# Kernel tuning notes

Hardware: AMD Instinct MI355X
Metric: run time of the kernel (lower is better)

The kernel has to match this reference:

```python
import jax, jax.numpy as jnp
import numpy as np

T_HID, A_HID, V_HID = 256, 128, 128
LEN = T_HID + A_HID + V_HID            # 512
TIME_WINDOW = 2
EXT_DIM = TIME_WINDOW * LEN + 1        # 1025
RANK, OUT_DIM = 128, 16
STRIDE = 2
B, T = 256, 128
T_IN, A_IN, V_IN = 768, 74, 35


def _mk_lstm(key, d_in, h):
    k1, k2, k3 = jax.random.split(key, 3)
    s = 1.0 / np.sqrt(h)
    W_ih = jax.random.uniform(k1, (4 * h, d_in), jnp.float32, -s, s)
    W_hh = jax.random.uniform(k2, (4 * h, h), jnp.float32, -s, s)
    b = jax.random.uniform(k3, (4 * h,), jnp.float32, -s, s)
    return W_ih, W_hh, b


def setup_inputs() -> dict:
    key = jax.random.key(0)
    ks = jax.random.split(key, 10)
    inp = {
        "text_x": jax.random.normal(ks[0], (B, T, T_IN), jnp.float32),
        "audio_x": jax.random.normal(ks[1], (B, T, A_IN), jnp.float32),
        "video_x": jax.random.normal(ks[2], (B, T, V_IN), jnp.float32),
    }
    inp["W_ih_t"], inp["W_hh_t"], inp["b_t"] = _mk_lstm(ks[3], T_IN, T_HID)
    inp["W_ih_a"], inp["W_hh_a"], inp["b_a"] = _mk_lstm(ks[4], A_IN, A_HID)
    inp["W_ih_v"], inp["W_hh_v"], inp["b_v"] = _mk_lstm(ks[5], V_IN, V_HID)
    ro = RANK * OUT_DIM
    inp["W1"] = jax.random.normal(ks[6], (ro, LEN), jnp.float32) / np.sqrt(LEN)
    inp["b1"] = jnp.zeros((ro,), jnp.float32)
    inp["W2"] = jax.random.normal(ks[7], (ro, EXT_DIM), jnp.float32) / np.sqrt(EXT_DIM)
    inp["b2"] = jnp.zeros((ro,), jnp.float32)
    inp["fusion_w"] = jax.random.normal(ks[8], (1, RANK), jnp.float32) * np.sqrt(2.0 / (1 + RANK))
    return inp


def _lstm(x, W_ih, W_hh, b, h):
    # x: [B,T,D] -> all hidden states [B,T,H]; PyTorch gate order i,f,g,o
    xp = jnp.einsum('btd,gd->btg', x, W_ih) + b  # [B,T,4H]
    h0 = jnp.zeros((x.shape[0], h), x.dtype)

    def step(carry, xt):
        hp, cp = carry
        g = xt + hp @ W_hh.T
        i, f, gg, o = jnp.split(g, 4, axis=-1)
        c = jax.nn.sigmoid(f) * cp + jax.nn.sigmoid(i) * jnp.tanh(gg)
        hn = jax.nn.sigmoid(o) * jnp.tanh(c)
        return (hn, c), hn

    _, hs = jax.lax.scan(step, (h0, h0), jnp.swapaxes(xp, 0, 1))
    return jnp.swapaxes(hs, 0, 1)


def reference(text_x, audio_x, video_x,
              W_ih_t, W_hh_t, b_t, W_ih_a, W_hh_a, b_a, W_ih_v, W_hh_v, b_v,
              W1, b1, W2, b2, fusion_w):
    audio_h = _lstm(audio_x, W_ih_a, W_hh_a, b_a, A_HID)
    video_h = _lstm(video_x, W_ih_v, W_hh_v, b_v, V_HID)
    text_h = _lstm(text_x, W_ih_t, W_hh_t, b_t, T_HID)
    z = jnp.concatenate((audio_h, video_h, text_h), axis=2)  # [B,T,LEN]

    # time_extend with circular wraparound: [B,T,1+W*LEN]
    tidx = (jnp.arange(T)[:, None] + jnp.arange(TIME_WINDOW)[None, :]) % T  # [T,W]
    z_ext = z[:, tidx, :].reshape(z.shape[0], T, TIME_WINDOW * LEN)
    ones = jnp.ones((z.shape[0], T, 1), z.dtype)
    z_ext = jnp.concatenate((ones, z_ext), axis=2)  # [B,T,EXT_DIM]

    idx = jnp.arange(0, T, STRIDE)  # strided fusion steps
    zi = z[:, idx, :]               # [B,K,LEN]
    ze = z_ext[:, idx, :]           # [B,K,EXT_DIM]
    f1 = jnp.einsum('bkd,rd->bkr', zi, W1) + b1
    f2 = jnp.einsum('bkd,rd->bkr', ze, W2) + b2
    z_fusion = jnp.mean(f1 * f2, axis=1)  # sum_i (.)/len(idx)  -> [B, RANK*OUT]
    z_fusion = z_fusion.reshape(-1, RANK, OUT_DIM)
    output = jnp.einsum('r,bro->bo', fusion_w[0], z_fusion)
    return output
```

## Files before the change

### kernel.cpp

```cpp
#include <hip/hip_runtime.h>
#include <hip/hip_bf16.h>
#include <math.h>


typedef __attribute__((ext_vector_type(8))) short short8;
typedef __attribute__((ext_vector_type(4))) float f32x4;

__device__ __forceinline__ float sigm(float x) { return 1.0f / (1.0f + __expf(-x)); }
__device__ __forceinline__ float tanh_(float x) {
    float ax = fabsf(x);
    float e  = __expf(-2.0f * ax);
    float t  = (1.0f - e) / (1.0f + e);
    return copysignf(t, x);
}
__device__ __forceinline__ ushort f2bf(float x) {
    __hip_bfloat16 h = __float2bfloat16(x);
    return *reinterpret_cast<ushort*>(&h);
}
__device__ __forceinline__ float bf2f(ushort u) { return __uint_as_float(((unsigned)u) << 16); }

__device__ __forceinline__ void gl_lds16(const void* g, void* l) {
    __builtin_amdgcn_global_load_lds(
        (const __attribute__((address_space(1))) unsigned int*)g,
        (__attribute__((address_space(3))) unsigned int*)l, 16, 0, 0);
}

#define BARRIER_LIGHT() \
    do { asm volatile("s_waitcnt lgkmcnt(0)" ::: "memory"); \
         __builtin_amdgcn_s_barrier(); \
         asm volatile("" ::: "memory"); } while (0)

__global__ void cvt_bf16(const float* __restrict__ src, ushort* __restrict__ dst,
                         int n8)
{
    int i = blockIdx.x * 256 + threadIdx.x;
    if (i >= n8) return;
    float4 a = ((const float4*)src)[2 * i];
    float4 b = ((const float4*)src)[2 * i + 1];
    short8 o;
    o[0] = f2bf(a.x); o[1] = f2bf(a.y); o[2] = f2bf(a.z); o[3] = f2bf(a.w);
    o[4] = f2bf(b.x); o[5] = f2bf(b.y); o[6] = f2bf(b.z); o[7] = f2bf(b.w);
    ((short8*)dst)[i] = o;
}

__global__ __launch_bounds__(256) void gemm_mfma_b(
    const ushort* __restrict__ A, const ushort* __restrict__ W,
    const float* __restrict__ bias, ushort* __restrict__ C,
    int M, int N, int K)
{
    constexpr int STR = 40;
    __shared__ ushort As[128 * STR];
    __shared__ ushort Ws[128 * STR];

    const int tid  = threadIdx.x;
    const int lane = tid & 63;
    const int wave = tid >> 6;
    const int bm   = blockIdx.y * 128;
    const int bn   = blockIdx.x * 128;
    const int m0   = (wave >> 1) * 64;
    const int n0   = (wave & 1) * 64;
    const int row  = tid >> 1;
    const int kseg = (tid & 1) * 16;
    const int fr   = lane & 15;
    const int fk   = (lane >> 4) * 8;

    f32x4 acc[4][4];
#pragma unroll
    for (int i = 0; i < 4; ++i)
#pragma unroll
        for (int j = 0; j < 4; ++j) acc[i][j] = (f32x4)(0.f);

    const bool kvec = (K & 7) == 0;

    for (int k0 = 0; k0 < K; k0 += 32) {
        {
            const ushort* ap = A + (size_t)(bm + row) * K + k0 + kseg;
            if (kvec && (k0 + kseg + 16) <= K) {
                *(int4*)&As[row * STR + kseg]     = *(const int4*)ap;
                *(int4*)&As[row * STR + kseg + 8] = *(const int4*)(ap + 8);
            } else {
#pragma unroll
                for (int j = 0; j < 16; ++j) {
                    int kk = k0 + kseg + j;
                    As[row * STR + kseg + j] = (kk < K) ? ap[j] : (ushort)0;
                }
            }
        }
        {
            const ushort* wp = W + (size_t)(bn + row) * K + k0 + kseg;
            if (kvec && (k0 + kseg + 16) <= K) {
                *(int4*)&Ws[row * STR + kseg]     = *(const int4*)wp;
                *(int4*)&Ws[row * STR + kseg + 8] = *(const int4*)(wp + 8);
            } else {
#pragma unroll
                for (int j = 0; j < 16; ++j) {
                    int kk = k0 + kseg + j;
                    Ws[row * STR + kseg + j] = (kk < K) ? wp[j] : (ushort)0;
                }
            }
        }
        __syncthreads();

        short8 af[4], wf[4];
#pragma unroll
        for (int mi = 0; mi < 4; ++mi)
            af[mi] = *(const short8*)&As[(m0 + mi * 16 + fr) * STR + fk];
#pragma unroll
        for (int ni = 0; ni < 4; ++ni)
            wf[ni] = *(const short8*)&Ws[(n0 + ni * 16 + fr) * STR + fk];
#pragma unroll
        for (int mi = 0; mi < 4; ++mi)
#pragma unroll
            for (int ni = 0; ni < 4; ++ni)
                acc[mi][ni] = __builtin_amdgcn_mfma_f32_16x16x32_bf16(
                    af[mi], wf[ni], acc[mi][ni], 0, 0, 0);
        __syncthreads();
    }

#pragma unroll
    for (int ni = 0; ni < 4; ++ni) {
        const int col = bn + n0 + ni * 16 + fr;
        const float bb = bias[col];
#pragma unroll
        for (int mi = 0; mi < 4; ++mi)
#pragma unroll
            for (int q = 0; q < 4; ++q) {
                int r  = bm + m0 + mi * 16 + (lane >> 4) * 4 + q;
                int b  = r >> 7, t = r & 127;
                size_t idx;
                if (N == 1024) {
                    int g = col >> 8, w = (col >> 5) & 7, s = (col >> 4) & 1, pl = col & 15;
                    idx = ((((size_t)(b >> 4) * 128 + t) * 8 + w) * 8 + (g * 2 + s)) * 256
                        + (size_t)(b & 15) * 16 + pl;
                } else {
                    int g = col >> 7, wq = (col >> 4) & 7, pl = col & 15;
                    idx = ((((size_t)(b >> 4) * 128 + t) * 8 + wq) * 4 + g) * 256
                        + (size_t)(b & 15) * 16 + pl;
                }
                C[idx] = f2bf(acc[mi][ni][q] + bb);
            }
    }
}

__global__ void wfrag_pack(const float* __restrict__ Wt, const float* __restrict__ Wa,
                           const float* __restrict__ Wv, ushort* __restrict__ WFt,
                           ushort* __restrict__ WFa, ushort* __restrict__ WFv)
{
    int idx = blockIdx.x * 256 + threadIdx.x;
    if (idx < 262144) {
        int e = idx;
        int jj = e & 7, n = (e >> 3) & 15, k8 = (e >> 7) & 3;
        int ti = e >> 9;
        int gs = ti & 7, w = (ti >> 3) & 7, kt = ti >> 6;
        int g = gs >> 1, s = gs & 1;
        WFt[e] = f2bf(Wt[(size_t)(g * 256 + w * 32 + s * 16 + n) * 256 + kt * 32 + k8 * 8 + jj]);
    } else if (idx < 327680) {
        int e = idx - 262144;
        int jj = e & 7, k8 = (e >> 3) & 3, n = (e >> 5) & 15;
        int g = (e >> 9) & 3, w = (e >> 11) & 7, kt = (e >> 14) & 3;
        WFa[e] = f2bf(Wa[(size_t)(g * 128 + w * 16 + n) * 128 + kt * 32 + k8 * 8 + jj]);
    } else if (idx < 393216) {
        int e = idx - 327680;
        int jj = e & 7, k8 = (e >> 3) & 3, n = (e >> 5) & 15;
        int g = (e >> 9) & 3, w = (e >> 11) & 7, kt = (e >> 14) & 3;
        WFv[e] = f2bf(Wv[(size_t)(g * 128 + w * 16 + n) * 128 + kt * 32 + k8 * 8 + jj]);
    }
}

__global__ void wf_pack(const float* __restrict__ W1, const float* __restrict__ W2,
                        ushort* __restrict__ W1b, ushort* __restrict__ W2ab,
                        ushort* __restrict__ W2bb)
{
    int idx = blockIdx.x * 256 + threadIdx.x;
    if (idx >= 1048576) return;
    int r = idx >> 9, c = idx & 511;
    W1b[idx]  = f2bf(W1[idx]);
    W2ab[idx] = f2bf(W2[(size_t)r * 1025 + 1 + c]);
    W2bb[idx] = f2bf(W2[(size_t)r * 1025 + 513 + c]);
}

#define STAGE_W(KT)                                                                \
    do {                                                                           \
        const char* gs_ = (const char*)WFt + (size_t)(((KT) * 8 + w) * 8) * 1024   \
                          + lane * 16;                                             \
        char* ld_ = wbuf + ((KT) & 1) * 8192;                                      \
        _Pragma("unroll") for (int e_ = 0; e_ < 8; ++e_)                           \
            gl_lds16(gs_ + e_ * 1024, ld_ + e_ * 1024);                            \
    } while (0)

#define TEXT_STEP(T, XC, XN, RP)                                                   \
    do {                                                                           \
        f32x4 acc[8];                                                              \
        _Pragma("unroll") for (int e = 0; e < 8; ++e) acc[e] = (f32x4)(0.f);       \
        _Pragma("unroll") for (int kt = 0; kt < 8; ++kt) {                         \
            if (kt < 2) { asm volatile("s_waitcnt vmcnt(16)" ::: "memory"); }      \
            else        { asm volatile("s_waitcnt vmcnt(8)" ::: "memory"); }       \
            __builtin_amdgcn_sched_barrier(0);                                     \
            short8 wt[8];                                                          \
            _Pragma("unroll") for (int e = 0; e < 8; ++e)                          \
                wt[e] = *(const short8*)(wbuf + (kt & 1) * 8192 + e * 1024 + lane * 16); \
            short8 hfk;                                                           \
            { int byt = (RP) * 8192 + np * 512 + kt * 64 + k8 * 16;                \
              hfk = *(const short8*)(hbase + (byt ^ ((np & 7) << 4))); }           \
            asm volatile("s_waitcnt lgkmcnt(0)" ::: "memory");                     \
            __builtin_amdgcn_sched_barrier(0);                                     \
            STAGE_W((kt + 2) & 7);                                                 \
            __builtin_amdgcn_sched_barrier(0);                                     \
            _Pragma("unroll") for (int e = 0; e < 8; ++e)                          \
                acc[e] = __builtin_amdgcn_mfma_f32_16x16x32_bf16(wt[e], hfk, acc[e], 0, 0, 0); \
        }                                                                          \
        _Pragma("unroll") for (int e = 0; e < 8; ++e) {                            \
            acc[e][0] += bf2f((ushort)((XC)[e].x & 0xffffu));                      \
            acc[e][1] += bf2f((ushort)((XC)[e].x >> 16));                          \
            acc[e][2] += bf2f((ushort)((XC)[e].y & 0xffffu));                      \
            acc[e][3] += bf2f((ushort)((XC)[e].y >> 16));                          \
        }                                                                          \
        uint2 hw[2];                                                               \
        _Pragma("unroll") for (int s = 0; s < 2; ++s) {                            \
            ushort hq[4];                                                          \
            _Pragma("unroll") for (int q = 0; q < 4; ++q) {                        \
                float iv = acc[0 + s][q], fv = acc[2 + s][q];                      \
                float gv = acc[4 + s][q], ov = acc[6 + s][q];                      \
                float cc = sigm(fv) * c_st[s][q] + sigm(iv) * tanh_(gv);           \
                c_st[s][q] = cc;                                                   \
                hq[q] = f2bf(sigm(ov) * tanh_(cc));                                \
            }                                                                      \
            hw[s].x = (uint)hq[0] | ((uint)hq[1] << 16);                           \
            hw[s].y = (uint)hq[2] | ((uint)hq[3] << 16);                           \
        }                                                                          \
        __builtin_amdgcn_sched_barrier(0);                                         \
        _Pragma("unroll") for (int s = 0; s < 2; ++s) {                            \
            int byt = ((RP) ^ 1) * 8192 + np * 512 + w * 64 + s * 32 + k8 * 8;     \
            *(uint2*)(hbase + (byt ^ ((np & 7) << 4))) = hw[s];                    \
            *(uint2*)(zb + zrow + (size_t)(T) * 512 + s * 16) = hw[s];             \
        }                                                                          \
        { const ushort* xrn = xbase + (size_t)(((T) + 1) & 127) * 16384;           \
          _Pragma("unroll") for (int e = 0; e < 8; ++e)                            \
              (XN)[e] = *(const uint2*)(xrn + e * 256); }                          \
        __builtin_amdgcn_sched_barrier(0);                                         \
        BARRIER_LIGHT();                                                           \
    } while (0)

#define AV_STEP(T, XC, XN, RP)                                                     \
    do {                                                                           \
        short8 hf[4];                                                              \
        _Pragma("unroll") for (int kt = 0; kt < 4; ++kt) {                         \
            int byt = (RP) * 4096 + np * 256 + kt * 64 + k8 * 16;                  \
            hf[kt] = *(const short8*)(hbase + (byt ^ ((np & 7) << 4)));            \
        }                                                                          \
        f32x4 acc[4];                                                              \
        _Pragma("unroll") for (int g = 0; g < 4; ++g) acc[g] = (f32x4)(0.f);       \
        _Pragma("unroll") for (int kt = 0; kt < 4; ++kt)                           \
            _Pragma("unroll") for (int g = 0; g < 4; ++g)                          \
                acc[g] = __builtin_amdgcn_mfma_f32_16x16x32_bf16(wres[kt][g], hf[kt], acc[g], 0, 0, 0); \
        { const ushort* xrn = xbase + (size_t)(((T) + 1) & 127) * 8192;            \
          _Pragma("unroll") for (int g = 0; g < 4; ++g)                            \
              (XN)[g] = *(const uint2*)(xrn + g * 256); }                          \
        _Pragma("unroll") for (int g = 0; g < 4; ++g) {                            \
            acc[g][0] += bf2f((ushort)((XC)[g].x & 0xffffu));                      \
            acc[g][1] += bf2f((ushort)((XC)[g].x >> 16));                          \
            acc[g][2] += bf2f((ushort)((XC)[g].y & 0xffffu));                      \
            acc[g][3] += bf2f((ushort)((XC)[g].y >> 16));                          \
        }                                                                          \
        ushort hq[4];                                                              \
        _Pragma("unroll") for (int q = 0; q < 4; ++q) {                            \
            float cc = sigm(acc[1][q]) * c_st0[q] + sigm(acc[0][q]) * tanh_(acc[2][q]); \
            c_st0[q] = cc;                                                         \
            hq[q] = f2bf(sigm(acc[3][q]) * tanh_(cc));                             \
        }                                                                          \
        uint2 hw;                                                                  \
        hw.x = (uint)hq[0] | ((uint)hq[1] << 16);                                  \
        hw.y = (uint)hq[2] | ((uint)hq[3] << 16);                                  \
        {                                                                          \
            int byt = ((RP) ^ 1) * 4096 + np * 256 + w * 32 + k8 * 8;              \
            *(uint2*)(hbase + (byt ^ ((np & 7) << 4))) = hw;                       \
            *(uint2*)(zb + zrow + (size_t)(T) * 512) = hw;                         \
        }                                                                          \
        BARRIER_LIGHT();                                                           \
    } while (0)

__global__ __launch_bounds__(512) void lstm_mfma5(
    const ushort* __restrict__ xpt, const ushort* __restrict__ xpa,
    const ushort* __restrict__ xpv, const ushort* __restrict__ WFt,
    const ushort* __restrict__ WFa, const ushort* __restrict__ WFv,
    ushort* __restrict__ zb)
{
    __shared__ __align__(16) char smem[147456];
    const int tid  = threadIdx.x;
    const int lane = tid & 63;
    const int w    = tid >> 6;
    const int np   = lane & 15;
    const int k8   = lane >> 4;
    const int bid  = blockIdx.x;
    char* hbase = smem;
    char* wbuf  = smem + 16384 + w * 16384;

    if (bid < 16) {
        const int bt = bid;
        const ushort* xbase = xpt + (size_t)bt * 2097152 + w * 2048 + np * 16 + k8 * 4;
        const size_t  zrow  = ((size_t)(bt * 16 + np) * 128) * 512 + 256 + w * 32 + k8 * 4;

        STAGE_W(0);
        STAGE_W(1);
        uint2 xvA[8], xvB[8];
#pragma unroll
        for (int e = 0; e < 8; ++e) xvA[e] = *(const uint2*)(xbase + e * 256);

        for (int i = tid; i < 4096; i += 512) ((uint*)hbase)[i] = 0u;
        float c_st[2][4];
#pragma unroll
        for (int s = 0; s < 2; ++s)
#pragma unroll
            for (int q = 0; q < 4; ++q) c_st[s][q] = 0.f;
        __syncthreads();

#pragma unroll 1
        for (int t = 0; t < 128; t += 2) {
            TEXT_STEP(t,     xvA, xvB, 0);
            TEXT_STEP(t + 1, xvB, xvA, 1);
        }
    } else {
        const bool isA = bid < 32;
        const int bt = bid - (isA ? 16 : 32);
        const ushort* xp = isA ? xpa : xpv;
        const ushort* WF = isA ? WFa : WFv;
        const int zoff = isA ? 0 : 128;

        short8 wres[4][4];
#pragma unroll
        for (int kt = 0; kt < 4; ++kt)
#pragma unroll
            for (int g = 0; g < 4; ++g)
                wres[kt][g] = *(const short8*)(WF + (size_t)((kt * 8 + w) * 4 + g) * 512 + np * 32 + k8 * 8);
        for (int i = tid; i < 2048; i += 512) ((uint*)hbase)[i] = 0u;
        float c_st0[4];
#pragma unroll
        for (int q = 0; q < 4; ++q) c_st0[q] = 0.f;
        __syncthreads();

        const ushort* xbase = xp + (size_t)bt * 1048576 + w * 1024 + np * 16 + k8 * 4;
        const size_t  zrow  = ((size_t)(bt * 16 + np) * 128) * 512 + zoff + w * 16 + k8 * 4;

        uint2 xvA[4], xvB[4];
#pragma unroll
        for (int g = 0; g < 4; ++g) xvA[g] = *(const uint2*)(xbase + g * 256);

#pragma unroll 1
        for (int t = 0; t < 128; t += 2) {
            AV_STEP(t,     xvA, xvB, 0);
            AV_STEP(t + 1, xvB, xvA, 1);
        }
    }
}

__global__ __launch_bounds__(256) void fuse_mfma(
    const ushort* __restrict__ zb, const ushort* __restrict__ W1b,
    const ushort* __restrict__ W2ab, const ushort* __restrict__ W2bb,
    const float* __restrict__ b1, const float* __restrict__ b2,
    const float* __restrict__ W2, float* __restrict__ zf)
{
    constexpr int STR = 40;
    __shared__ ushort As[64 * STR];
    __shared__ ushort W1s[256 * STR];
    __shared__ ushort W2s[256 * STR];

    const int tid  = threadIdx.x;
    const int lane = tid & 63;
    const int wave = tid >> 6;
    const int b    = blockIdx.y;
    const int r0   = blockIdx.x * 256;
    const int n0w  = wave * 64;

    const int a_row  = tid >> 2;
    const int a_c8   = (tid & 3) * 8;
    const int fr_row = lane & 15;
    const int fr_k   = (lane >> 4) * 8;

    f32x4 acc1[4][4], acc2[4][4];
#pragma unroll
    for (int i = 0; i < 4; ++i)
#pragma unroll
        for (int j = 0; j < 4; ++j) {
            acc1[i][j] = (f32x4)(0.f);
            acc2[i][j] = (f32x4)(0.f);
        }

    for (int pass = 0; pass < 2; ++pass) {
        const ushort* wsrc = pass ? W2bb : W2ab;
        for (int c0 = 0; c0 < 512; c0 += 32) {
            {
                const int4 v = *(const int4*)(zb +
                    (((size_t)b * 128 + 2 * a_row + pass) * 512 + c0 + a_c8));
                *(int4*)&As[a_row * STR + a_c8] = v;
            }
            if (pass == 0) {
                const ushort* w1p = W1b + (size_t)(r0 + tid) * 512 + c0;
#pragma unroll
                for (int j = 0; j < 4; ++j)
                    *(int4*)&W1s[tid * STR + j * 8] = *(const int4*)(w1p + j * 8);
            }
            {
                const ushort* w2p = wsrc + (size_t)(r0 + tid) * 512 + c0;
#pragma unroll
                for (int j = 0; j < 4; ++j)
                    *(int4*)&W2s[tid * STR + j * 8] = *(const int4*)(w2p + j * 8);
            }
            __syncthreads();

            short8 af[4], w2f[4];
#pragma unroll
            for (int mi = 0; mi < 4; ++mi)
                af[mi] = *(const short8*)&As[(mi * 16 + fr_row) * STR + fr_k];
#pragma unroll
            for (int ni = 0; ni < 4; ++ni)
                w2f[ni] = *(const short8*)&W2s[(n0w + ni * 16 + fr_row) * STR + fr_k];

            if (pass == 0) {
                short8 w1f[4];
#pragma unroll
                for (int ni = 0; ni < 4; ++ni)
                    w1f[ni] = *(const short8*)&W1s[(n0w + ni * 16 + fr_row) * STR + fr_k];
#pragma unroll
                for (int mi = 0; mi < 4; ++mi)
#pragma unroll
                    for (int ni = 0; ni < 4; ++ni) {
                        acc1[mi][ni] = __builtin_amdgcn_mfma_f32_16x16x32_bf16(
                            af[mi], w1f[ni], acc1[mi][ni], 0, 0, 0);
                        acc2[mi][ni] = __builtin_amdgcn_mfma_f32_16x16x32_bf16(
                            af[mi], w2f[ni], acc2[mi][ni], 0, 0, 0);
                    }
            } else {
#pragma unroll
                for (int mi = 0; mi < 4; ++mi)
#pragma unroll
                    for (int ni = 0; ni < 4; ++ni)
                        acc2[mi][ni] = __builtin_amdgcn_mfma_f32_16x16x32_bf16(
                            af[mi], w2f[ni], acc2[mi][ni], 0, 0, 0);
            }
            __syncthreads();
        }
    }

#pragma unroll
    for (int ni = 0; ni < 4; ++ni) {
        const int r = r0 + n0w + ni * 16 + fr_row;
        const float bb1 = b1[r];
        const float bb2 = b2[r] + W2[(size_t)r * 1025];
        float s = 0.f;
#pragma unroll
        for (int mi = 0; mi < 4; ++mi)
#pragma unroll
            for (int q = 0; q < 4; ++q)
                s += (acc1[mi][ni][q] + bb1) * (acc2[mi][ni][q] + bb2);
        s += __shfl_xor(s, 16);
        s += __shfl_xor(s, 32);
        if ((lane >> 4) == 0)
            zf[(size_t)b * 2048 + r] = s * (1.0f / 64.0f);
    }
}

__global__ void final_out(const float* __restrict__ zf, const float* __restrict__ fw,
                          float* __restrict__ out)
{
    int idx = blockIdx.x * 256 + threadIdx.x;
    int b = idx >> 4, o = idx & 15;
    float s = 0.f;
#pragma unroll
    for (int r = 0; r < 128; ++r)
        s = fmaf(fw[r], zf[(size_t)b * 2048 + r * 16 + o], s);
    out[idx] = s;
}

extern "C" void kernel_launch(void* const* d_in, const int* in_sizes, int n_in,
                              void* d_out, int out_size, void* d_ws, size_t ws_size,
                              hipStream_t stream)
{
    const float* text_x  = (const float*)d_in[0];
    const float* audio_x = (const float*)d_in[1];
    const float* video_x = (const float*)d_in[2];
    const float* W_ih_t  = (const float*)d_in[3];
    const float* W_hh_t  = (const float*)d_in[4];
    const float* b_t     = (const float*)d_in[5];
    const float* W_ih_a  = (const float*)d_in[6];
    const float* W_hh_a  = (const float*)d_in[7];
    const float* b_a     = (const float*)d_in[8];
    const float* W_ih_v  = (const float*)d_in[9];
    const float* W_hh_v  = (const float*)d_in[10];
    const float* b_v     = (const float*)d_in[11];
    const float* W1      = (const float*)d_in[12];
    const float* b1      = (const float*)d_in[13];
    const float* W2      = (const float*)d_in[14];
    const float* b2      = (const float*)d_in[15];
    const float* fw      = (const float*)d_in[16];
    float* out = (float*)d_out;

    char* base = (char*)d_ws;
    ushort* xpt  = (ushort*)(base);
    ushort* xpa  = (ushort*)(base + 67108864);
    ushort* xpv  = (ushort*)(base + 100663296);
    ushort* zbuf = (ushort*)(base + 134217728);
    ushort* WFt  = (ushort*)(base + 167772160);
    ushort* WFa  = (ushort*)(base + 168296448);
    ushort* WFv  = (ushort*)(base + 168427520);
    ushort* W1b  = (ushort*)(base + 168558592);
    ushort* W2ab = (ushort*)(base + 170655744);
    ushort* W2bb = (ushort*)(base + 172752896);
    float*  zf   = (float*)(base + 174850048);
    ushort* txb  = (ushort*)(base + 176947200);
    ushort* axb  = (ushort*)(base + 227278848);
    ushort* vxb  = (ushort*)(base + 232128512);
    ushort* wtb  = (ushort*)(base + 234422272);
    ushort* wab  = (ushort*)(base + 235995136);
    ushort* wvb  = (ushort*)(base + 236070912);

    cvt_bf16<<<(3145728 + 255) / 256, 256, 0, stream>>>(text_x,  txb, 3145728);
    cvt_bf16<<<(303104  + 255) / 256, 256, 0, stream>>>(audio_x, axb, 303104);
    cvt_bf16<<<(143360  + 255) / 256, 256, 0, stream>>>(video_x, vxb, 143360);
    cvt_bf16<<<(98304   + 255) / 256, 256, 0, stream>>>(W_ih_t,  wtb, 98304);
    cvt_bf16<<<(4736    + 255) / 256, 256, 0, stream>>>(W_ih_a,  wab, 4736);
    cvt_bf16<<<(2240    + 255) / 256, 256, 0, stream>>>(W_ih_v,  wvb, 2240);

    gemm_mfma_b<<<dim3(8, 256), 256, 0, stream>>>(txb, wtb, b_t, xpt, 32768, 1024, 768);
    gemm_mfma_b<<<dim3(4, 256), 256, 0, stream>>>(axb, wab, b_a, xpa, 32768, 512, 74);
    gemm_mfma_b<<<dim3(4, 256), 256, 0, stream>>>(vxb, wvb, b_v, xpv, 32768, 512, 35);
    wfrag_pack<<<1536, 256, 0, stream>>>(W_hh_t, W_hh_a, W_hh_v, WFt, WFa, WFv);
    wf_pack<<<4096, 256, 0, stream>>>(W1, W2, W1b, W2ab, W2bb);
    lstm_mfma5<<<48, 512, 0, stream>>>(xpt, xpa, xpv, WFt, WFa, WFv, zbuf);
    fuse_mfma<<<dim3(8, 256), 256, 0, stream>>>(zbuf, W1b, W2ab, W2bb, b1, b2, W2, zf);
    final_out<<<16, 256, 0, stream>>>(zf, fw, out);
}
```

Measured before the change: 1.592 ms.

## Load text LSTM recurrent weights directly from global instead of LDS staging; merge converts

The text LSTM step now reads W_hh fragments straight from global memory (L2-resident) into registers rather than staging them into LDS via async global_load_lds double buffering with explicit vmcnt waits. This shrinks shared memory from 144KB to 16KB and removes the staging waits and barriers. In exchange, each step incurs global/L2 load latency on the critical recurrent path. Separately, six fp32-to-bf16 conversion launches are merged into one kernel to cut launch overhead.

```diff
diff --git a/kernel.cpp b/kernel.cpp
--- a/kernel.cpp
+++ b/kernel.cpp
@@ -19,28 +19,33 @@
 }
 __device__ __forceinline__ float bf2f(ushort u) { return __uint_as_float(((unsigned)u) << 16); }
 
-__device__ __forceinline__ void gl_lds16(const void* g, void* l) {
-    __builtin_amdgcn_global_load_lds(
-        (const __attribute__((address_space(1))) unsigned int*)g,
-        (__attribute__((address_space(3))) unsigned int*)l, 16, 0, 0);
-}
-
 #define BARRIER_LIGHT() \
     do { asm volatile("s_waitcnt lgkmcnt(0)" ::: "memory"); \
          __builtin_amdgcn_s_barrier(); \
          asm volatile("" ::: "memory"); } while (0)
 
-__global__ void cvt_bf16(const float* __restrict__ src, ushort* __restrict__ dst,
-                         int n8)
+__global__ void cvt_all(const float* __restrict__ t, const float* __restrict__ a,
+                        const float* __restrict__ v, const float* __restrict__ wt,
+                        const float* __restrict__ wa, const float* __restrict__ wv,
+                        ushort* __restrict__ td, ushort* __restrict__ ad,
+                        ushort* __restrict__ vd, ushort* __restrict__ wtd,
+                        ushort* __restrict__ wad, ushort* __restrict__ wvd)
 {
     int i = blockIdx.x * 256 + threadIdx.x;
-    if (i >= n8) return;
-    float4 a = ((const float4*)src)[2 * i];
-    float4 b = ((const float4*)src)[2 * i + 1];
+    const float* s; ushort* d; int off;
+    if (i < 3145728)      { s = t;  d = td;  off = i; }
+    else if (i < 3448832) { s = a;  d = ad;  off = i - 3145728; }
+    else if (i < 3592192) { s = v;  d = vd;  off = i - 3448832; }
+    else if (i < 3690496) { s = wt; d = wtd; off = i - 3592192; }
+    else if (i < 3695232) { s = wa; d = wad; off = i - 3690496; }
+    else if (i < 3697472) { s = wv; d = wvd; off = i - 3695232; }
+    else return;
+    float4 A = ((const float4*)s)[2 * off];
+    float4 B = ((const float4*)s)[2 * off + 1];
     short8 o;
-    o[0] = f2bf(a.x); o[1] = f2bf(a.y); o[2] = f2bf(a.z); o[3] = f2bf(a.w);
-    o[4] = f2bf(b.x); o[5] = f2bf(b.y); o[6] = f2bf(b.z); o[7] = f2bf(b.w);
-    ((short8*)dst)[i] = o;
+    o[0] = f2bf(A.x); o[1] = f2bf(A.y); o[2] = f2bf(A.z); o[3] = f2bf(A.w);
+    o[4] = f2bf(B.x); o[5] = f2bf(B.y); o[6] = f2bf(B.z); o[7] = f2bf(B.w);
+    ((short8*)d)[off] = o;
 }
 
 __global__ __launch_bounds__(256) void gemm_mfma_b(
@@ -179,36 +184,22 @@
     W2bb[idx] = f2bf(W2[(size_t)r * 1025 + 513 + c]);
 }
 
-#define STAGE_W(KT)                                                                \
-    do {                                                                           \
-        const char* gs_ = (const char*)WFt + (size_t)(((KT) * 8 + w) * 8) * 1024   \
-                          + lane * 16;                                             \
-        char* ld_ = wbuf + ((KT) & 1) * 8192;                                      \
-        _Pragma("unroll") for (int e_ = 0; e_ < 8; ++e_)                           \
-            gl_lds16(gs_ + e_ * 1024, ld_ + e_ * 1024);                            \
-    } while (0)
-
 #define TEXT_STEP(T, XC, XN, RP)                                                   \
     do {                                                                           \
         f32x4 acc[8];                                                              \
         _Pragma("unroll") for (int e = 0; e < 8; ++e) acc[e] = (f32x4)(0.f);       \
         _Pragma("unroll") for (int kt = 0; kt < 8; ++kt) {                         \
-            if (kt < 2) { asm volatile("s_waitcnt vmcnt(16)" ::: "memory"); }      \
-            else        { asm volatile("s_waitcnt vmcnt(8)" ::: "memory"); }       \
             __builtin_amdgcn_sched_barrier(0);                                     \
             short8 wt[8];                                                          \
             _Pragma("unroll") for (int e = 0; e < 8; ++e)                          \
-                wt[e] = *(const short8*)(wbuf + (kt & 1) * 8192 + e * 1024 + lane * 16); \
-            short8 hfk;                                                           \
+                wt[e] = *(const short8*)(wthr + (size_t)(kt * 64 + e) * 512);      \
+            short8 hfk;                                                            \
             { int byt = (RP) * 8192 + np * 512 + kt * 64 + k8 * 16;                \
               hfk = *(const short8*)(hbase + (byt ^ ((np & 7) << 4))); }           \
-            asm volatile("s_waitcnt lgkmcnt(0)" ::: "memory");                     \
-            __builtin_amdgcn_sched_barrier(0);                                     \
-            STAGE_W((kt + 2) & 7);                                                 \
-            __builtin_amdgcn_sched_barrier(0);                                     \
             _Pragma("unroll") for (int e = 0; e < 8; ++e)                          \
                 acc[e] = __builtin_amdgcn_mfma_f32_16x16x32_bf16(wt[e], hfk, acc[e], 0, 0, 0); \
         }                                                                          \
+        __builtin_amdgcn_sched_barrier(0);                                         \
         _Pragma("unroll") for (int e = 0; e < 8; ++e) {                            \
             acc[e][0] += bf2f((ushort)((XC)[e].x & 0xffffu));                      \
             acc[e][1] += bf2f((ushort)((XC)[e].x >> 16));                          \
@@ -228,7 +219,6 @@
             hw[s].x = (uint)hq[0] | ((uint)hq[1] << 16);                           \
             hw[s].y = (uint)hq[2] | ((uint)hq[3] << 16);                           \
         }                                                                          \
-        __builtin_amdgcn_sched_barrier(0);                                         \
         _Pragma("unroll") for (int s = 0; s < 2; ++s) {                            \
             int byt = ((RP) ^ 1) * 8192 + np * 512 + w * 64 + s * 32 + k8 * 8;     \
             *(uint2*)(hbase + (byt ^ ((np & 7) << 4))) = hw[s];                    \
@@ -237,7 +227,6 @@
         { const ushort* xrn = xbase + (size_t)(((T) + 1) & 127) * 16384;           \
           _Pragma("unroll") for (int e = 0; e < 8; ++e)                            \
               (XN)[e] = *(const uint2*)(xrn + e * 256); }                          \
-        __builtin_amdgcn_sched_barrier(0);                                         \
         BARRIER_LIGHT();                                                           \
     } while (0)
 
@@ -279,13 +268,13 @@
         BARRIER_LIGHT();                                                           \
     } while (0)
 
-__global__ __launch_bounds__(512) void lstm_mfma5(
+__global__ __launch_bounds__(512) void lstm_mfma7(
     const ushort* __restrict__ xpt, const ushort* __restrict__ xpa,
     const ushort* __restrict__ xpv, const ushort* __restrict__ WFt,
     const ushort* __restrict__ WFa, const ushort* __restrict__ WFv,
     ushort* __restrict__ zb)
 {
-    __shared__ __align__(16) char smem[147456];
+    __shared__ __align__(16) char smem[16384];
     const int tid  = threadIdx.x;
     const int lane = tid & 63;
     const int w    = tid >> 6;
@@ -293,15 +282,13 @@
     const int k8   = lane >> 4;
     const int bid  = blockIdx.x;
     char* hbase = smem;
-    char* wbuf  = smem + 16384 + w * 16384;
 
     if (bid < 16) {
         const int bt = bid;
         const ushort* xbase = xpt + (size_t)bt * 2097152 + w * 2048 + np * 16 + k8 * 4;
+        const ushort* wthr  = WFt + (size_t)(w * 8) * 512 + k8 * 128 + np * 8;
         const size_t  zrow  = ((size_t)(bt * 16 + np) * 128) * 512 + 256 + w * 32 + k8 * 4;
 
-        STAGE_W(0);
-        STAGE_W(1);
         uint2 xvA[8], xvB[8];
 #pragma unroll
         for (int e = 0; e < 8; ++e) xvA[e] = *(const uint2*)(xbase + e * 256);
@@ -513,19 +500,15 @@
     ushort* wab  = (ushort*)(base + 235995136);
     ushort* wvb  = (ushort*)(base + 236070912);
 
-    cvt_bf16<<<(3145728 + 255) / 256, 256, 0, stream>>>(text_x,  txb, 3145728);
-    cvt_bf16<<<(303104  + 255) / 256, 256, 0, stream>>>(audio_x, axb, 303104);
-    cvt_bf16<<<(143360  + 255) / 256, 256, 0, stream>>>(video_x, vxb, 143360);
-    cvt_bf16<<<(98304   + 255) / 256, 256, 0, stream>>>(W_ih_t,  wtb, 98304);
-    cvt_bf16<<<(4736    + 255) / 256, 256, 0, stream>>>(W_ih_a,  wab, 4736);
-    cvt_bf16<<<(2240    + 255) / 256, 256, 0, stream>>>(W_ih_v,  wvb, 2240);
+    cvt_all<<<14444, 256, 0, stream>>>(text_x, audio_x, video_x, W_ih_t, W_ih_a, W_ih_v,
+                                       txb, axb, vxb, wtb, wab, wvb);
 
     gemm_mfma_b<<<dim3(8, 256), 256, 0, stream>>>(txb, wtb, b_t, xpt, 32768, 1024, 768);
     gemm_mfma_b<<<dim3(4, 256), 256, 0, stream>>>(axb, wab, b_a, xpa, 32768, 512, 74);
     gemm_mfma_b<<<dim3(4, 256), 256, 0, stream>>>(vxb, wvb, b_v, xpv, 32768, 512, 35);
     wfrag_pack<<<1536, 256, 0, stream>>>(W_hh_t, W_hh_a, W_hh_v, WFt, WFa, WFv);
     wf_pack<<<4096, 256, 0, stream>>>(W1, W2, W1b, W2ab, W2bb);
-    lstm_mfma5<<<48, 512, 0, stream>>>(xpt, xpa, xpv, WFt, WFa, WFv, zbuf);
+    lstm_mfma7<<<48, 512, 0, stream>>>(xpt, xpa, xpv, WFt, WFa, WFv, zbuf);
     fuse_mfma<<<dim3(8, 256), 256, 0, stream>>>(zbuf, W1b, W2ab, W2bb, b1, b2, W2, zf);
     final_out<<<16, 256, 0, stream>>>(zf, fw, out);
 }
```

Result: slower. 2.181 ms (+37.1%).
